# Performance work log

Hardware: AMD Instinct MI355X
Metric: run time of the kernel (lower is better)

The kernel has to match this reference:

```python
import jax, jax.numpy as jnp
import numpy as np

B, S, D_IN, D, H = 2, 2048, 1024, 1024, 16
HD = D // H

def setup_inputs() -> dict:
    key = jax.random.key(0)
    k1, k2, k3 = jax.random.split(key, 3)
    # xavier_uniform-style scale for weights
    lim_qkv = float(np.sqrt(6.0 / (D_IN + 3 * D)))
    lim_o = float(np.sqrt(6.0 / (D + D)))
    return {
        "x": jax.random.normal(k1, (B, S, D_IN), dtype=jnp.float32),
        "w_qkv": jax.random.uniform(k2, (3 * D, D_IN), dtype=jnp.float32, minval=-lim_qkv, maxval=lim_qkv),
        "b_qkv": jnp.zeros((3 * D,), dtype=jnp.float32),
        "w_o": jax.random.uniform(k3, (D, D), dtype=jnp.float32, minval=-lim_o, maxval=lim_o),
        "b_o": jnp.zeros((D,), dtype=jnp.float32),
    }

def reference(x, w_qkv, b_qkv, w_o, b_o):
    b, s, _ = x.shape
    # QKV projection: [B,S,3D]
    qkv = jnp.einsum("bsd,ed->bse", x, w_qkv) + b_qkv
    # [B,S,H,3*HD] -> [B,H,S,3*HD]
    qkv = qkv.reshape(b, s, H, 3 * HD).transpose(0, 2, 1, 3)
    q, k, v = jnp.split(qkv, 3, axis=-1)  # each [B,H,S,HD]
    scale = 1.0 / jnp.sqrt(jnp.asarray(HD, dtype=q.dtype))
    logits = jnp.einsum("bhqd,bhkd->bhqk", q, k) * scale  # [B,H,S,S]
    attn = jax.nn.softmax(logits, axis=-1)
    vals = jnp.einsum("bhqk,bhkd->bhqd", attn, v)  # [B,H,S,HD]
    vals = vals.transpose(0, 2, 1, 3).reshape(b, s, D)
    return jnp.einsum("bsd,ed->bse", vals, w_o) + b_o
```

## Files before the change

### kernel.cpp

```cpp
#include <hip/hip_runtime.h>
#include <hip/hip_bf16.h>
#include <math.h>

#define BATCH 2
#define SLEN  2048
#define DIN   1024
#define DMODEL 1024
#define NHEAD 16
#define HD    64
#define E3    3072

typedef unsigned short us;
typedef _Float16 f16;
typedef __attribute__((ext_vector_type(8))) _Float16 f16x8;
typedef __attribute__((ext_vector_type(8))) unsigned short us8;
typedef __attribute__((ext_vector_type(4))) unsigned short us4;
typedef __attribute__((ext_vector_type(4))) float f32x4;
typedef __attribute__((ext_vector_type(16))) float f32x16;
typedef __attribute__((ext_vector_type(4))) unsigned int u32x4;

#define QSCALE 0.18033688011112042f

__device__ __forceinline__ us f16bits(float x) {
    const f16 h = (f16)x;
    return __builtin_bit_cast(us, h);
}

__device__ __forceinline__ unsigned int pkrtz(float a, float b) {
    return __builtin_bit_cast(unsigned int, __builtin_amdgcn_cvt_pkrtz(a, b));
}

__device__ __forceinline__ void plswap(unsigned int& a, unsigned int& b) {
    asm volatile("v_permlane32_swap_b32 %0, %1" : "+v"(a), "+v"(b));
}

__device__ __forceinline__ void barrier_raw() {
    asm volatile("s_barrier" ::: "memory");
}

#define GLL16(g, l)                                                                     \
    __builtin_amdgcn_global_load_lds((const __attribute__((address_space(1))) unsigned int*)(g), \
                                     (__attribute__((address_space(3))) unsigned int*)(l), 16, 0, 0)

__global__ __launch_bounds__(256) void cvt3_f16(
    const float* __restrict__ x, us* __restrict__ ox, int nx,
    const float* __restrict__ wq, us* __restrict__ owq, int nq,
    const float* __restrict__ wo, us* __restrict__ owo)
{
    int i = (blockIdx.x * 256 + threadIdx.x) * 8;
    const float* s;
    us* o;
    if (i < nx)           { s = x;  o = ox; }
    else if (i < nx + nq) { s = wq; o = owq; i -= nx; }
    else                  { s = wo; o = owo; i -= nx + nq; }
    const float4 f0 = *(const float4*)&s[i];
    const float4 f1 = *(const float4*)&s[i + 4];
    const float v[8] = {f0.x, f0.y, f0.z, f0.w, f1.x, f1.y, f1.z, f1.w};
    us8 h;
#pragma unroll
    for (int j = 0; j < 8; ++j) h[j] = f16bits(v[j]);
    *(us8*)&o[i] = h;
}

#define GBK 64
#define GNT (DIN / GBK)

template <int BN, bool QKV_OUT>
__global__ __launch_bounds__(256) void gemm_db(
    const us* __restrict__ Am, const us* __restrict__ Bm,
    const float* __restrict__ bias, void* __restrict__ Cout,
    int M, int N, int K)
{
    constexpr int NJ  = BN / 32;
    constexpr int BGL = BN / 32;
    __shared__ __align__(16) us ldsA[2 * 128 * 64];
    __shared__ __align__(16) us ldsB[2 * BN * 64];

    const int t    = threadIdx.x;
    const int lane = t & 63;
    const int w    = t >> 6;
    const int ml   = lane & 15;
    const int quad = lane >> 4;
    const int msk  = ml & 7;
    const int wm   = w >> 1;
    const int wn   = w & 1;

    const int nbx = N / BN;
    const int nwg = (M >> 7) * nbx;
    int wg = blockIdx.y * nbx + blockIdx.x;
    wg = (wg & 7) * (nwg >> 3) + (wg >> 3);
    const int m0 = (wg / nbx) * 128;
    const int n0 = (wg % nbx) * BN;

    const int r8  = lane >> 3;
    const int xsw = ((lane & 7) ^ r8) * 8;
    const us* pA = Am + (size_t)(m0 + w * 32 + r8) * K + xsw;
    const int brow = (BN == 128) ? w * 32 : w * 16;
    const us* pB = Bm + (size_t)(n0 + brow + r8) * K + xsw;

#define STG_A(d, kk) do { _Pragma("unroll") for (int g = 0; g < 4; ++g) \
    GLL16(pA + (size_t)(8 * g) * K + (kk), &ldsA[(d) * 8192 + w * 2048 + g * 512]); } while (0)
#define STG_B(d, kk) do { _Pragma("unroll") for (int g = 0; g < BGL; ++g) \
    GLL16(pB + (size_t)(8 * g) * K + (kk), &ldsB[(d) * (BN * 64) + brow * 64 + g * 512]); } while (0)

#define LDA(d, mi, ks) __builtin_bit_cast(f16x8, *(const us8*)&ldsA[(d) * 8192 + (wm * 64 + (mi) * 16 + ml) * 64 + (((quad ^ msk) ^ ((ks) << 2)) * 8)])
#define LDB(d, nj, ks) __builtin_bit_cast(f16x8, *(const us8*)&ldsB[(d) * (BN * 64) + (wn * (BN / 2) + (nj) * 16 + ml) * 64 + (((quad ^ msk) ^ ((ks) << 2)) * 8)])

#define WAIT_BGL() do { if constexpr (BN == 128) asm volatile("s_waitcnt vmcnt(4)" ::: "memory"); \
                        else                     asm volatile("s_waitcnt vmcnt(2)" ::: "memory"); } while (0)

    f32x4 acc[4][NJ];
#pragma unroll
    for (int i = 0; i < 4; ++i)
#pragma unroll
        for (int j = 0; j < NJ; ++j) {
            acc[i][j][0] = 0.f; acc[i][j][1] = 0.f; acc[i][j][2] = 0.f; acc[i][j][3] = 0.f;
        }

    STG_A(0, 0); STG_B(0, 0);
    STG_B(1, GBK);
    WAIT_BGL();
    barrier_raw();

    for (int tt = 0; tt < GNT; ++tt) {
        const int d = tt & 1, e = d ^ 1;

        if (tt + 1 < GNT) STG_A(e, (tt + 1) * GBK);
        f16x8 bf[2][NJ];
#pragma unroll
        for (int ks = 0; ks < 2; ++ks)
#pragma unroll
            for (int nj = 0; nj < NJ; ++nj)
                bf[ks][nj] = LDB(d, nj, ks);
        f16x8 a0[2][2];
#pragma unroll
        for (int mi = 0; mi < 2; ++mi) {
            a0[mi][0] = LDA(d, mi, 0);
            a0[mi][1] = LDA(d, mi, 1);
        }
        __builtin_amdgcn_s_setprio(1);
#pragma unroll
        for (int ks = 0; ks < 2; ++ks)
#pragma unroll
            for (int nj = 0; nj < NJ; ++nj)
#pragma unroll
                for (int mi = 0; mi < 2; ++mi)
                    acc[mi][nj] = __builtin_amdgcn_mfma_f32_16x16x32_f16(a0[mi][ks], bf[ks][nj], acc[mi][nj], 0, 0, 0);
        __builtin_amdgcn_s_setprio(0);
        barrier_raw();

        if (tt + 2 < GNT) STG_B(d, (tt + 2) * GBK);
        f16x8 a1[2][2];
#pragma unroll
        for (int mi = 0; mi < 2; ++mi) {
            a1[mi][0] = LDA(d, mi + 2, 0);
            a1[mi][1] = LDA(d, mi + 2, 1);
        }
        __builtin_amdgcn_s_setprio(1);
#pragma unroll
        for (int ks = 0; ks < 2; ++ks)
#pragma unroll
            for (int nj = 0; nj < NJ; ++nj)
#pragma unroll
                for (int mi = 0; mi < 2; ++mi)
                    acc[mi + 2][nj] = __builtin_amdgcn_mfma_f32_16x16x32_f16(a1[mi][ks], bf[ks][nj], acc[mi + 2][nj], 0, 0, 0);
        __builtin_amdgcn_s_setprio(0);

        if (tt + 2 < GNT)      WAIT_BGL();
        else if (tt + 1 < GNT) asm volatile("s_waitcnt vmcnt(0)" ::: "memory");
        barrier_raw();
    }

    float bj[NJ], cs[NJ];
#pragma unroll
    for (int nj = 0; nj < NJ; ++nj) {
        const int col = n0 + wn * (BN / 2) + nj * 16 + ml;
        bj[nj] = bias[col];
        cs[nj] = (QKV_OUT && (col % 192) < 64) ? QSCALE : 1.0f;
    }
#pragma unroll
    for (int mi = 0; mi < 4; ++mi) {
#pragma unroll
        for (int r = 0; r < 4; ++r) {
            const size_t rowoff = (size_t)(m0 + wm * 64 + mi * 16 + quad * 4 + r) * N;
#pragma unroll
            for (int nj = 0; nj < NJ; ++nj) {
                const int col = n0 + wn * (BN / 2) + nj * 16 + ml;
                const float v = (acc[mi][nj][r] + bj[nj]) * cs[nj];
                if (QKV_OUT) ((us*)Cout)[rowoff + col] = f16bits(v);
                else         ((float*)Cout)[rowoff + col] = v;
            }
        }
    }
#undef STG_A
#undef STG_B
#undef LDA
#undef LDB
#undef WAIT_BGL
}

#define ABQ 128
#define ACH 64
#define NCH (SLEN / ACH)
#define NCH2 (NCH / 2)
#define LQA 72
#define OSTR 68

__global__ __launch_bounds__(512, 4) void attn_mfma(
    const us* __restrict__ qkvh, us* __restrict__ vals)
{
    __shared__ __align__(16) us smem[18432];
    us* const Ks = smem;
    us* const Vt = smem + 9216;

    const int t    = threadIdx.x;
    const int lane = t & 63;
    const int w    = t >> 6;
    const int sp   = w >> 2;
    const int wq4  = w & 3;
    const int t2   = t & 255;
    const int m32  = lane & 31;
    const int half = lane >> 5;

    const int wg  = blockIdx.x;
    const int s9  = wg >> 3;
    const int bh  = ((s9 >> 4) << 3) | (wg & 7);
    const int b   = bh >> 4;
    const int h   = bh & 15;
    const int q0  = (s9 & 15) * ABQ;

    const size_t base = (size_t)b * SLEN * E3;
    const int qoff = h * 192;

    const int krA = t2 >> 2;
    const int ksA = (t2 & 3) * 16;
    const int k2  = t2 & 31;
    const int d0v = (t2 >> 5) * 8;

    us* const myK = Ks + sp * 4608;
    us* const myV = Vt + sp * 4608;
    const int cg0 = sp * NCH2;

    us8 kk0, kk1, vv0, vv1;
    {
        const us* gK = &qkvh[base + (size_t)(cg0 * ACH + krA) * E3 + qoff + 64 + ksA];
        kk0 = *(const us8*)gK; kk1 = *(const us8*)(gK + 8);
        const us* gV = &qkvh[base + (size_t)(cg0 * ACH + 2 * k2) * E3 + qoff + 128 + d0v];
        vv0 = *(const us8*)gV; vv1 = *(const us8*)(gV + E3);
    }

    {
        const int row = t >> 2;
        const int c0q = (t & 3) * 16;
        const us* g = &qkvh[base + (size_t)(q0 + row) * E3 + qoff + c0q];
        *(us8*)&smem[row * LQA + c0q]     = *(const us8*)g;
        *(us8*)&smem[row * LQA + c0q + 8] = *(const us8*)(g + 8);
    }
    __syncthreads();

    f16x8 aq[4];
#pragma unroll
    for (int s = 0; s < 4; ++s)
        aq[s] = __builtin_bit_cast(f16x8, *(const us8*)&smem[(wq4 * 32 + m32) * LQA + half * 8 + 16 * s]);

    f32x16 O[2];
#pragma unroll
    for (int dt = 0; dt < 2; ++dt)
#pragma unroll
        for (int r = 0; r < 16; ++r) O[dt][r] = 0.f;
    float lp[2] = {0.f, 0.f};

    for (int c = 0; c < NCH2; ++c) {
        __syncthreads();
        *(us8*)&myK[krA * LQA + ksA]     = kk0;
        *(us8*)&myK[krA * LQA + ksA + 8] = kk1;
#pragma unroll
        for (int j = 0; j < 8; ++j) {
            const unsigned int pv = (unsigned int)vv0[j] | ((unsigned int)vv1[j] << 16);
            *(unsigned int*)&myV[(d0v + j) * LQA + 2 * k2] = pv;
        }
        __syncthreads();
        if (c + 1 < NCH2) {
            const int cg = cg0 + c + 1;
            const us* gK = &qkvh[base + (size_t)(cg * ACH + krA) * E3 + qoff + 64 + ksA];
            kk0 = *(const us8*)gK; kk1 = *(const us8*)(gK + 8);
            const us* gV = &qkvh[base + (size_t)(cg * ACH + 2 * k2) * E3 + qoff + 128 + d0v];
            vv0 = *(const us8*)gV; vv1 = *(const us8*)(gV + E3);
        }

        f16x8 pf[4];
#pragma unroll
        for (int kt = 0; kt < 2; ++kt) {
            f32x16 z;
#pragma unroll
            for (int r = 0; r < 16; ++r) z[r] = 0.f;
#pragma unroll
            for (int s = 0; s < 4; ++s) {
                const f16x8 ak = __builtin_bit_cast(f16x8, *(const us8*)&myK[(kt * 32 + m32) * LQA + half * 8 + 16 * s]);
                z = __builtin_amdgcn_mfma_f32_32x32x16_f16(ak, aq[s], z, 0, 0, 0);
            }
            {
                float p[8];
#pragma unroll
                for (int r = 0; r < 8; ++r) {
                    p[r] = __builtin_amdgcn_exp2f(z[r]);
                    lp[r & 1] += p[r];
                }
                unsigned int a0 = pkrtz(p[0], p[1]), a1 = pkrtz(p[2], p[3]);
                unsigned int b0 = pkrtz(p[4], p[5]), b1 = pkrtz(p[6], p[7]);
                plswap(a0, b0); plswap(a1, b1);
                pf[2 * kt] = __builtin_bit_cast(f16x8, (u32x4){a0, a1, b0, b1});
            }
            {
                float p[8];
#pragma unroll
                for (int r = 0; r < 8; ++r) {
                    p[r] = __builtin_amdgcn_exp2f(z[8 + r]);
                    lp[r & 1] += p[r];
                }
                unsigned int e0 = pkrtz(p[0], p[1]), e1 = pkrtz(p[2], p[3]);
                unsigned int f0 = pkrtz(p[4], p[5]), f1 = pkrtz(p[6], p[7]);
                plswap(e0, f0); plswap(e1, f1);
                pf[2 * kt + 1] = __builtin_bit_cast(f16x8, (u32x4){e0, e1, f0, f1});
            }
        }

#pragma unroll
        for (int dt = 0; dt < 2; ++dt) {
#pragma unroll
            for (int s = 0; s < 4; ++s) {
                const f16x8 av = __builtin_bit_cast(f16x8, *(const us8*)&myV[(dt * 32 + m32) * LQA + half * 8 + 16 * s]);
                O[dt] = __builtin_amdgcn_mfma_f32_32x32x16_f16(av, pf[s], O[dt], 0, 0, 0);
            }
        }
    }

    const float lpart = lp[0] + lp[1];
    const float l = lpart + __shfl_xor(lpart, 32);
    const int ql = wq4 * 32 + m32;

    __syncthreads();
    float* const Osc = (float*)smem;
    float* const lsc = Osc + ABQ * OSTR;

    if (sp == 1) {
#pragma unroll
        for (int dt = 0; dt < 2; ++dt) {
#pragma unroll
            for (int g = 0; g < 4; ++g) {
                const f32x4 o4 = {O[dt][g * 4], O[dt][g * 4 + 1], O[dt][g * 4 + 2], O[dt][g * 4 + 3]};
                *(f32x4*)&Osc[ql * OSTR + dt * 32 + 8 * g + 4 * half] = o4;
            }
        }
        if (half == 0) lsc[ql] = l;
    }
    __syncthreads();
    if (sp == 0) {
        const float rl = 1.0f / (l + lsc[ql]);
        const int sq = q0 + ql;
        const size_t rowbase = (size_t)(b * SLEN + sq) * DMODEL + h * HD;
#pragma unroll
        for (int dt = 0; dt < 2; ++dt) {
#pragma unroll
            for (int g = 0; g < 4; ++g) {
                const f32x4 part = *(const f32x4*)&Osc[ql * OSTR + dt * 32 + 8 * g + 4 * half];
                us4 o4;
#pragma unroll
                for (int r2 = 0; r2 < 4; ++r2)
                    o4[r2] = f16bits((O[dt][g * 4 + r2] + part[r2]) * rl);
                *(us4*)&vals[rowbase + dt * 32 + 8 * g + 4 * half] = o4;
            }
        }
    }
}

extern "C" void kernel_launch(void* const* d_in, const int* in_sizes, int n_in,
                              void* d_out, int out_size, void* d_ws, size_t ws_size,
                              hipStream_t stream) {
    const float* x     = (const float*)d_in[0];
    const float* w_qkv = (const float*)d_in[1];
    const float* b_qkv = (const float*)d_in[2];
    const float* w_o   = (const float*)d_in[3];
    const float* b_o   = (const float*)d_in[4];
    float* out = (float*)d_out;

    const int M   = BATCH * SLEN;
    const int XN  = M * DIN;
    const int WQN = E3 * DIN;
    const int WON = DMODEL * DMODEL;
    const size_t QKVN = (size_t)BATCH * SLEN * E3;

    us* qkvh = (us*)d_ws;
    us* xh   = qkvh + QKVN;
    us* wq   = xh + XN;
    us* wo   = wq + WQN;

    cvt3_f16<<<dim3((XN + WQN + WON) / 2048), 256, 0, stream>>>(
        x, xh, XN, w_qkv, wq, WQN, w_o, wo);

    gemm_db<128, true><<<dim3(E3 / 128, M / 128), 256, 0, stream>>>(
        xh, wq, b_qkv, qkvh, M, E3, DIN);

    us* vals = xh;
    attn_mfma<<<dim3((SLEN / ABQ) * BATCH * NHEAD), 512, 0, stream>>>(qkvh, vals);

    gemm_db<64, false><<<dim3(DMODEL / 64, M / 128), 256, 0, stream>>>(
        vals, wo, b_o, out, M, DMODEL, DMODEL);
}
```

Measured before the change: 185.9 us.

## Double-buffer K/V tiles in LDS and raise MFMA wave priority in attention

The attention kernel now holds two LDS buffers for K and V. The next chunk is written to LDS while the current chunk is consumed, which cuts the two barriers per iteration down to one, and global prefetch runs two chunks ahead. s_setprio brackets the MFMA sections so waves issuing matrix ops get priority. The cost is that LDS use doubles to 72KB per block and launch bounds drop to 2 blocks per CU, which may reduce occupancy.

Result: no change. 189.0 us (+1.6%).

```diff
diff --git a/kernel.cpp b/kernel.cpp
--- a/kernel.cpp
+++ b/kernel.cpp
@@ -206,12 +206,10 @@
 #define LQA 72
 #define OSTR 68
 
-__global__ __launch_bounds__(512, 4) void attn_mfma(
+__global__ __launch_bounds__(512, 2) void attn_mfma(
     const us* __restrict__ qkvh, us* __restrict__ vals)
 {
-    __shared__ __align__(16) us smem[18432];
-    us* const Ks = smem;
-    us* const Vt = smem + 9216;
+    __shared__ __align__(16) us smem[36864];
 
     const int t    = threadIdx.x;
     const int lane = t & 63;
@@ -237,18 +235,20 @@
     const int k2  = t2 & 31;
     const int d0v = (t2 >> 5) * 8;
 
-    us* const myK = Ks + sp * 4608;
-    us* const myV = Vt + sp * 4608;
+    us* const Kb0 = smem + sp * 4608;
+    us* const Kb1 = smem + 9216 + sp * 4608;
+    us* const Vb0 = smem + 18432 + sp * 4608;
+    us* const Vb1 = smem + 27648 + sp * 4608;
     const int cg0 = sp * NCH2;
 
     us8 kk0, kk1, vv0, vv1;
-    {
-        const us* gK = &qkvh[base + (size_t)(cg0 * ACH + krA) * E3 + qoff + 64 + ksA];
-        kk0 = *(const us8*)gK; kk1 = *(const us8*)(gK + 8);
-        const us* gV = &qkvh[base + (size_t)(cg0 * ACH + 2 * k2) * E3 + qoff + 128 + d0v];
-        vv0 = *(const us8*)gV; vv1 = *(const us8*)(gV + E3);
-    }
-
+#define LOADKV(cgi) do { \
+    const us* gK = &qkvh[base + (size_t)((cgi) * ACH + krA) * E3 + qoff + 64 + ksA]; \
+    kk0 = *(const us8*)gK; kk1 = *(const us8*)(gK + 8); \
+    const us* gV = &qkvh[base + (size_t)((cgi) * ACH + 2 * k2) * E3 + qoff + 128 + d0v]; \
+    vv0 = *(const us8*)gV; vv1 = *(const us8*)(gV + E3); } while (0)
+
+    LOADKV(cg0);
     {
         const int row = t >> 2;
         const int c0q = (t & 3) * 16;
@@ -262,6 +262,17 @@
 #pragma unroll
     for (int s = 0; s < 4; ++s)
         aq[s] = __builtin_bit_cast(f16x8, *(const us8*)&smem[(wq4 * 32 + m32) * LQA + half * 8 + 16 * s]);
+    __syncthreads();
+
+    *(us8*)&Kb0[krA * LQA + ksA]     = kk0;
+    *(us8*)&Kb0[krA * LQA + ksA + 8] = kk1;
+#pragma unroll
+    for (int j = 0; j < 8; ++j) {
+        const unsigned int pv = (unsigned int)vv0[j] | ((unsigned int)vv1[j] << 16);
+        *(unsigned int*)&Vb0[(d0v + j) * LQA + 2 * k2] = pv;
+    }
+    LOADKV(cg0 + 1);
+    __syncthreads();
 
     f32x16 O[2];
 #pragma unroll
@@ -271,22 +282,21 @@
     float lp[2] = {0.f, 0.f};
 
     for (int c = 0; c < NCH2; ++c) {
-        __syncthreads();
-        *(us8*)&myK[krA * LQA + ksA]     = kk0;
-        *(us8*)&myK[krA * LQA + ksA + 8] = kk1;
-#pragma unroll
-        for (int j = 0; j < 8; ++j) {
-            const unsigned int pv = (unsigned int)vv0[j] | ((unsigned int)vv1[j] << 16);
-            *(unsigned int*)&myV[(d0v + j) * LQA + 2 * k2] = pv;
-        }
-        __syncthreads();
+        us* const Krd = (c & 1) ? Kb1 : Kb0;
+        us* const Vrd = (c & 1) ? Vb1 : Vb0;
+        us* const Kwr = (c & 1) ? Kb0 : Kb1;
+        us* const Vwr = (c & 1) ? Vb0 : Vb1;
+
         if (c + 1 < NCH2) {
-            const int cg = cg0 + c + 1;
-            const us* gK = &qkvh[base + (size_t)(cg * ACH + krA) * E3 + qoff + 64 + ksA];
-            kk0 = *(const us8*)gK; kk1 = *(const us8*)(gK + 8);
-            const us* gV = &qkvh[base + (size_t)(cg * ACH + 2 * k2) * E3 + qoff + 128 + d0v];
-            vv0 = *(const us8*)gV; vv1 = *(const us8*)(gV + E3);
-        }
+            *(us8*)&Kwr[krA * LQA + ksA]     = kk0;
+            *(us8*)&Kwr[krA * LQA + ksA + 8] = kk1;
+#pragma unroll
+            for (int j = 0; j < 8; ++j) {
+                const unsigned int pv = (unsigned int)vv0[j] | ((unsigned int)vv1[j] << 16);
+                *(unsigned int*)&Vwr[(d0v + j) * LQA + 2 * k2] = pv;
+            }
+        }
+        if (c + 2 < NCH2) LOADKV(cg0 + c + 2);
 
         f16x8 pf[4];
 #pragma unroll
@@ -294,11 +304,13 @@
             f32x16 z;
 #pragma unroll
             for (int r = 0; r < 16; ++r) z[r] = 0.f;
+            __builtin_amdgcn_s_setprio(1);
 #pragma unroll
             for (int s = 0; s < 4; ++s) {
-                const f16x8 ak = __builtin_bit_cast(f16x8, *(const us8*)&myK[(kt * 32 + m32) * LQA + half * 8 + 16 * s]);
+                const f16x8 ak = __builtin_bit_cast(f16x8, *(const us8*)&Krd[(kt * 32 + m32) * LQA + half * 8 + 16 * s]);
                 z = __builtin_amdgcn_mfma_f32_32x32x16_f16(ak, aq[s], z, 0, 0, 0);
             }
+            __builtin_amdgcn_s_setprio(0);
             {
                 float p[8];
 #pragma unroll
@@ -325,14 +337,18 @@
             }
         }
 
+        __builtin_amdgcn_s_setprio(1);
 #pragma unroll
         for (int dt = 0; dt < 2; ++dt) {
 #pragma unroll
             for (int s = 0; s < 4; ++s) {
-                const f16x8 av = __builtin_bit_cast(f16x8, *(const us8*)&myV[(dt * 32 + m32) * LQA + half * 8 + 16 * s]);
+                const f16x8 av = __builtin_bit_cast(f16x8, *(const us8*)&Vrd[(dt * 32 + m32) * LQA + half * 8 + 16 * s]);
                 O[dt] = __builtin_amdgcn_mfma_f32_32x32x16_f16(av, pf[s], O[dt], 0, 0, 0);
             }
         }
+        __builtin_amdgcn_s_setprio(0);
+
+        __syncthreads();
     }
 
     const float lpart = lp[0] + lp[1];
@@ -372,6 +388,7 @@
             }
         }
     }
+#undef LOADKV
 }
 
 extern "C" void kernel_launch(void* const* d_in, const int* in_sizes, int n_in,
```
